# Kernel optimization log

Hardware: AMD Instinct MI355X
Metric: run time of the kernel (lower is better)

Reference implementation:

```python
import jax, jax.numpy as jnp
import numpy as np

L = 16384      # sequence length
D_IN = 512     # d_input
D_H = 1024     # d_hidden
D_OUT = 512    # d_output
R_MIN = 0.0
R_MAX = 0.99
MAX_PHASE = np.pi


def setup_inputs() -> dict:
    key = jax.random.key(0)
    k_nu, k_th, k_x, k_bre, k_bim, k_cre, k_cim, k_d = jax.random.split(key, 8)
    # nu_init with parametrization='exp'
    u_nu = jax.random.uniform(k_nu, (D_H,), dtype=jnp.float32)
    nu = jnp.sqrt(u_nu * (R_MAX ** 2 - R_MIN ** 2) + R_MIN ** 2)
    u_theta = jax.random.uniform(k_th, (D_H,), dtype=jnp.float32, minval=-MAX_PHASE, maxval=MAX_PHASE)
    theta = jnp.mod(u_theta, 2 * jnp.pi)
    lamb = jnp.stack([jnp.log(-jnp.log(nu)), jnp.log(theta)], axis=0)  # [2, D_H]
    # gamma_init with parametrization='exp': nu = exp(-exp(lamb[0]))
    nu_eff = jnp.exp(-jnp.exp(lamb[0]))
    gamma = jnp.log(jnp.sqrt(1.0 - jnp.abs(nu_eff) ** 2))  # [D_H]
    # matrix_init: normal / sqrt(shape[0])
    B_re = jax.random.normal(k_bre, (D_H, D_IN), dtype=jnp.float32) / jnp.sqrt(D_H)
    B_im = jax.random.normal(k_bim, (D_H, D_IN), dtype=jnp.float32) / jnp.sqrt(D_H)
    C_re = jax.random.normal(k_cre, (D_OUT, D_H), dtype=jnp.float32) / jnp.sqrt(D_OUT)
    C_im = jax.random.normal(k_cim, (D_OUT, D_H), dtype=jnp.float32) / jnp.sqrt(D_OUT)
    D = jax.random.normal(k_d, (D_OUT, D_IN), dtype=jnp.float32) / jnp.sqrt(D_OUT)
    inputs = jax.random.normal(k_x, (L, D_IN), dtype=jnp.float32)
    return {"inputs": inputs, "lamb": lamb, "gamma": gamma,
            "B_re": B_re, "B_im": B_im, "C_re": C_re, "C_im": C_im, "D": D}


def _binary_operator_diag(q_i, q_j):
    A_i, b_i = q_i
    A_j, b_j = q_j
    return (A_j * A_i, A_j * b_i + b_j)


def reference(inputs, lamb, gamma, B_re, B_im, C_re, C_im, D):
    # parametrization='exp': lambda = exp(-exp(nu_log) + i*exp(theta_log))
    diag_lambda = jnp.exp(-jnp.exp(lamb[0]) + 1j * jnp.exp(lamb[1]))  # [D_H] complex64
    # which_gamma='learned', exp param: scale rows of B by exp(gamma)
    B_norm = jnp.exp(gamma)[:, None] * (B_re + 1j * B_im)             # [D_H, D_IN]
    # Bu_t = B_norm @ x_t for all t, as one GEMM: [L, D_H] complex
    Bu = inputs.astype(B_norm.dtype) @ B_norm.T
    Lambda_elements = jnp.broadcast_to(diag_lambda[None, :], Bu.shape)
    # diagonal linear recurrence h_t = lambda*h_{t-1} + Bu_t via parallel scan
    _, h = jax.lax.associative_scan(_binary_operator_diag, (Lambda_elements, Bu))
    C = C_re + 1j * C_im
    # y_t = Re[C h_t] + D x_t
    outputs = jnp.real(h @ C.T) + inputs @ D.T  # [L, D_OUT]
    return outputs
```

## Files before the change

### kernel.cpp

```cpp
#include <hip/hip_runtime.h>

__device__ __forceinline__ unsigned short f2b(float f) {
    unsigned int u = __builtin_bit_cast(unsigned int, f);
    unsigned int r = (u + 0x7FFFu + ((u >> 16) & 1u)) >> 16;
    return (unsigned short)r;
}
__device__ __forceinline__ float b2f(unsigned short s) {
    unsigned int u = ((unsigned int)s) << 16;
    return __builtin_bit_cast(float, u);
}

typedef __attribute__((ext_vector_type(8))) short short8;
typedef __attribute__((ext_vector_type(4))) float float4v;

#define GLD16(g, l) __builtin_amdgcn_global_load_lds(                          \
    (const __attribute__((address_space(1))) unsigned int*)(g),                \
    (__attribute__((address_space(3))) unsigned int*)(l), 16, 0, 0)

#define WAIT_VMN(n)  __builtin_amdgcn_s_waitcnt(0x0F70 | (n))
#define SB()         __builtin_amdgcn_sched_barrier(0)
#define BAR()        __builtin_amdgcn_s_barrier()

#define SEQLEN 16384
#define NCHUNK 512
#define TCHUNK 32
#define LDH 2560

__global__ void prep_all(const float* __restrict__ x,
                         const float* __restrict__ B_re, const float* __restrict__ B_im,
                         const float* __restrict__ gamma,
                         const float* __restrict__ C_re, const float* __restrict__ C_im,
                         const float* __restrict__ Dm,
                         unsigned short* __restrict__ Hcat,
                         unsigned short* __restrict__ Bcat,
                         unsigned short* __restrict__ CW) {
    int b = blockIdx.x;
    if (b < 8192) {
        int id = b * 256 + threadIdx.x;
        int t = id >> 7;
        int k4 = (id & 127) << 2;
        float4 v = *(const float4*)(x + (long)t * 512 + k4);
        ushort4 o;
        o.x = f2b(v.x); o.y = f2b(v.y); o.z = f2b(v.z); o.w = f2b(v.w);
        *(ushort4*)(Hcat + (long)t * LDH + 2048 + k4) = o;
    } else if (b < 9216) {
        int id = (b - 8192) * 256 + threadIdx.x;
        int n = id >> 7;
        int k4 = (id & 127) << 2;
        const float* src = (n < 1024) ? (B_re + (long)n * 512) : (B_im + (long)(n - 1024) * 512);
        float g = expf(gamma[n & 1023]);
        float4 v = *(const float4*)(src + k4);
        ushort4 o;
        o.x = f2b(v.x * g); o.y = f2b(v.y * g); o.z = f2b(v.z * g); o.w = f2b(v.w * g);
        *(ushort4*)(Bcat + (long)n * 512 + k4) = o;
    } else {
        int id = (b - 9216) * 256 + threadIdx.x;
        int o = id / 640;
        int j4 = (id - o * 640) << 2;
        float4 v; float sgn = 1.0f;
        if (j4 < 1024) {
            v = *(const float4*)(C_re + (long)o * 1024 + j4);
        } else if (j4 < 2048) {
            v = *(const float4*)(C_im + (long)o * 1024 + (j4 - 1024));
            sgn = -1.0f;
        } else {
            v = *(const float4*)(Dm + (long)o * 512 + (j4 - 2048));
        }
        ushort4 w;
        w.x = f2b(v.x * sgn); w.y = f2b(v.y * sgn); w.z = f2b(v.z * sgn); w.w = f2b(v.w * sgn);
        *(ushort4*)(CW + (long)o * 2560 + j4) = w;
    }
}

__global__ __launch_bounds__(512, 1)
void gemm_bu(const unsigned short* __restrict__ A, int lda,
             const unsigned short* __restrict__ B, int ldb,
             unsigned short* __restrict__ Cout, int ldc) {
    constexpr int ASH = 16384;
    __shared__ unsigned short sm[2][32768] __attribute__((aligned(16)));

    const int tid  = threadIdx.x;
    const int lane = tid & 63;
    const int wid  = tid >> 6;
    const int wr   = wid >> 2;
    const int wc   = wid & 3;

    const int bid = blockIdx.x;
    const int l = (bid & 7) * 64 + (bid >> 3);
    const long m0 = (long)(l >> 3) * 256;
    const long n0 = (long)(l & 7) * 256;

    const int sr = lane >> 3;
    const int sc = ((lane & 7) ^ sr) << 3;
    const unsigned short* Agl = A + (m0 + sr) * (long)lda + sc;
    const unsigned short* Bgl = B + (n0 + sr) * (long)ldb + sc;

    const int fr = lane & 15;
    const int x7 = fr & 7;
    const int k0off = (((lane >> 4)    ) ^ x7) << 3;
    const int k1off = (((lane >> 4) + 4) ^ x7) << 3;

    float4v acc[8][4] = {};
    short8 fa[4][2];
    short8 fb[4][2];

    auto stageB = [&](unsigned short* buf, long kt) {
        unsigned short* ldsB = buf + ASH + wid * 512;
        const unsigned short* gB = Bgl + kt;
#pragma unroll
        for (int i = 0; i < 4; i++)
            GLD16(gB + (long)(8 * (wid + 8 * i)) * ldb, ldsB + i * 4096);
    };
    auto stageA = [&](unsigned short* buf, long kt) {
        unsigned short* ldsA = buf + wid * 512;
        const unsigned short* gA = Agl + kt;
#pragma unroll
        for (int i = 0; i < 4; i++)
            GLD16(gA + (long)(8 * (wid + 8 * i)) * lda, ldsA + i * 4096);
    };
    auto ldA = [&](const unsigned short* buf, int mbase) {
#pragma unroll
        for (int i = 0; i < 4; i++) {
            const unsigned short* p = buf + (wr * 128 + (mbase + i) * 16 + fr) * 64;
            fa[i][0] = *(const short8*)(p + k0off);
            fa[i][1] = *(const short8*)(p + k1off);
        }
    };
    auto ldB = [&](const unsigned short* buf, int nbase) {
#pragma unroll
        for (int j = 0; j < 2; j++) {
            const unsigned short* p = buf + ASH + (wc * 64 + (nbase + j) * 16 + fr) * 64;
            fb[nbase + j][0] = *(const short8*)(p + k0off);
            fb[nbase + j][1] = *(const short8*)(p + k1off);
        }
    };
    auto mfmaQ = [&](int mbase, int nbase) {
        __builtin_amdgcn_s_setprio(1);
#pragma unroll
        for (int i = 0; i < 4; i++)
#pragma unroll
            for (int j = 0; j < 2; j++) {
                acc[mbase + i][nbase + j] = __builtin_amdgcn_mfma_f32_16x16x32_bf16(
                    fa[i][0], fb[nbase + j][0], acc[mbase + i][nbase + j], 0, 0, 0);
                acc[mbase + i][nbase + j] = __builtin_amdgcn_mfma_f32_16x16x32_bf16(
                    fa[i][1], fb[nbase + j][1], acc[mbase + i][nbase + j], 0, 0, 0);
            }
        __builtin_amdgcn_s_setprio(0);
    };

    const int nk = 8;
    stageB(sm[0], 0);  stageA(sm[0], 0);
    stageB(sm[1], 64); stageA(sm[1], 64);
    WAIT_VMN(8);
    SB(); BAR(); SB();

    for (int t = 0; t < nk; ++t) {
        unsigned short* cur = sm[t & 1];
        const bool st = (t + 2 < nk);
        const long kt2 = (long)(t + 2) * 64;
        ldA(cur, 0); ldB(cur, 0);
        SB(); BAR(); SB();
        mfmaQ(0, 0);
        SB(); BAR(); SB();
        ldB(cur, 2);
        SB(); BAR(); SB();
        mfmaQ(0, 2);
        SB(); BAR(); SB();
        if (st) stageB(cur, kt2);
        ldA(cur, 4);
        SB(); BAR(); SB();
        mfmaQ(4, 0);
        SB(); BAR(); SB();
        if (st) stageA(cur, kt2);
        SB();
        mfmaQ(4, 2);
        if (st)              WAIT_VMN(8);
        else if (t + 1 < nk) WAIT_VMN(0);
        SB(); BAR(); SB();
    }

    const int er = (lane >> 4) * 4;
    const int ec = lane & 15;
#pragma unroll
    for (int mi = 0; mi < 8; mi++) {
#pragma unroll
        for (int r = 0; r < 4; r++) {
            long grow = m0 + wr * 128 + mi * 16 + er + r;
#pragma unroll
            for (int nj = 0; nj < 4; nj++) {
                long gcol = n0 + wc * 64 + nj * 16 + ec;
                Cout[grow * ldc + gcol] = f2b(acc[mi][nj][r]);
            }
        }
    }
}

__global__ __launch_bounds__(512, 1)
void gemm_y(const unsigned short* __restrict__ A, int lda,
            const unsigned short* __restrict__ B, int ldb,
            float* __restrict__ Cout, int ldc) {
    constexpr int ASH = 8192;
    __shared__ unsigned short sm[2][ASH + 16384] __attribute__((aligned(16)));

    const int tid  = threadIdx.x;
    const int lane = tid & 63;
    const int wid  = tid >> 6;
    const int wr   = wid >> 2;
    const int wc   = wid & 3;

    const int bid = blockIdx.x;
    const int xcd = bid & 7;
    const int g   = bid >> 3;
    const int bx  = g & 1;
    const int by  = xcd * 16 + (g >> 1);
    const long m0 = (long)by * 128;
    const long n0 = (long)bx * 256;

    const int sr = lane >> 3;
    const int sc = ((lane & 7) ^ sr) << 3;
    const unsigned short* Agl = A + (m0 + sr) * (long)lda + sc;
    const unsigned short* Bgl = B + (n0 + sr) * (long)ldb + sc;

    const int fr = lane & 15;
    const int x7 = fr & 7;
    const int k0off = (((lane >> 4)    ) ^ x7) << 3;
    const int k1off = (((lane >> 4) + 4) ^ x7) << 3;

    float4v acc[4][4] = {};
    short8 fa[2][2];
    short8 fb[4][2];

    auto stageB = [&](unsigned short* buf, long kt) {
        unsigned short* ldsB = buf + ASH + wid * 512;
        const unsigned short* gB = Bgl + kt;
#pragma unroll
        for (int i = 0; i < 4; i++)
            GLD16(gB + (long)(8 * (wid + 8 * i)) * ldb, ldsB + i * 4096);
    };
    auto stageA = [&](unsigned short* buf, long kt) {
        unsigned short* ldsA = buf + wid * 512;
        const unsigned short* gA = Agl + kt;
#pragma unroll
        for (int i = 0; i < 2; i++)
            GLD16(gA + (long)(8 * (wid + 8 * i)) * lda, ldsA + i * 4096);
    };
    auto ldA = [&](const unsigned short* buf, int mbase) {
#pragma unroll
        for (int i = 0; i < 2; i++) {
            const unsigned short* p = buf + (wr * 64 + (mbase + i) * 16 + fr) * 64;
            fa[i][0] = *(const short8*)(p + k0off);
            fa[i][1] = *(const short8*)(p + k1off);
        }
    };
    auto ldB = [&](const unsigned short* buf, int nbase) {
#pragma unroll
        for (int j = 0; j < 2; j++) {
            const unsigned short* p = buf + ASH + (wc * 64 + (nbase + j) * 16 + fr) * 64;
            fb[nbase + j][0] = *(const short8*)(p + k0off);
            fb[nbase + j][1] = *(const short8*)(p + k1off);
        }
    };
    auto mfmaQ = [&](int mbase, int nbase) {
        __builtin_amdgcn_s_setprio(1);
#pragma unroll
        for (int i = 0; i < 2; i++)
#pragma unroll
            for (int j = 0; j < 2; j++) {
                acc[mbase + i][nbase + j] = __builtin_amdgcn_mfma_f32_16x16x32_bf16(
                    fa[i][0], fb[nbase + j][0], acc[mbase + i][nbase + j], 0, 0, 0);
                acc[mbase + i][nbase + j] = __builtin_amdgcn_mfma_f32_16x16x32_bf16(
                    fa[i][1], fb[nbase + j][1], acc[mbase + i][nbase + j], 0, 0, 0);
            }
        __builtin_amdgcn_s_setprio(0);
    };

    const int nk = 40;
    stageB(sm[0], 0);  stageA(sm[0], 0);
    stageB(sm[1], 64); stageA(sm[1], 64);
    WAIT_VMN(6);
    SB(); BAR(); SB();

    for (int t = 0; t < nk; ++t) {
        unsigned short* cur = sm[t & 1];
        const bool st = (t + 2 < nk);
        const long kt2 = (long)(t + 2) * 64;
        ldA(cur, 0); ldB(cur, 0);
        SB(); BAR(); SB();
        mfmaQ(0, 0);
        SB(); BAR(); SB();
        ldB(cur, 2);
        SB(); BAR(); SB();
        mfmaQ(0, 2);
        SB(); BAR(); SB();
        if (st) stageB(cur, kt2);
        ldA(cur, 2);
        SB(); BAR(); SB();
        mfmaQ(2, 0);
        SB(); BAR(); SB();
        if (st) stageA(cur, kt2);
        SB();
        mfmaQ(2, 2);
        if (st)              WAIT_VMN(6);
        else if (t + 1 < nk) WAIT_VMN(0);
        SB(); BAR(); SB();
    }

    const int er = (lane >> 4) * 4;
    const int ec = lane & 15;
#pragma unroll
    for (int mi = 0; mi < 4; mi++) {
#pragma unroll
        for (int r = 0; r < 4; r++) {
            long grow = m0 + wr * 64 + mi * 16 + er + r;
#pragma unroll
            for (int nj = 0; nj < 4; nj++) {
                long gcol = n0 + wc * 64 + nj * 16 + ec;
                Cout[grow * ldc + gcol] = acc[mi][nj][r];
            }
        }
    }
}

__global__ void scan_ends(const unsigned short* __restrict__ Hcat,
                          const float* __restrict__ lamb,
                          float* __restrict__ E) {
    const int chunk = blockIdx.x;
    const int ch = threadIdx.x << 2;
    float lre[4], lim[4];
#pragma unroll
    for (int i = 0; i < 4; i++) {
        float nu = expf(-expf(lamb[ch + i]));
        float th = expf(lamb[1024 + ch + i]);
        lre[i] = nu * cosf(th);
        lim[i] = nu * sinf(th);
    }
    float hr[4] = {0, 0, 0, 0}, hi[4] = {0, 0, 0, 0};
    const unsigned short* base = Hcat + (long)chunk * TCHUNK * LDH + ch;
#pragma unroll 4
    for (int t = 0; t < TCHUNK; t++) {
        ushort4 br = *(const ushort4*)(base + (long)t * LDH);
        ushort4 bi = *(const ushort4*)(base + (long)t * LDH + 1024);
        float brf[4] = {b2f(br.x), b2f(br.y), b2f(br.z), b2f(br.w)};
        float bif[4] = {b2f(bi.x), b2f(bi.y), b2f(bi.z), b2f(bi.w)};
#pragma unroll
        for (int i = 0; i < 4; i++) {
            float nr = fmaf(lre[i], hr[i], fmaf(-lim[i], hi[i], brf[i]));
            float ni = fmaf(lre[i], hi[i], fmaf(lim[i], hr[i], bif[i]));
            hr[i] = nr; hi[i] = ni;
        }
    }
    float* Ec = E + (long)chunk * 2048 + ch;
#pragma unroll
    for (int i = 0; i < 4; i++) {
        Ec[i] = hr[i];
        Ec[1024 + i] = hi[i];
    }
}

__global__ void carry(const float* __restrict__ lamb, const float* __restrict__ E,
                      float* __restrict__ Kc) {
    const int lane = threadIdx.x & 63;
    const int ch = blockIdx.x * 4 + (threadIdx.x >> 6);
    double nu = exp(-exp((double)lamb[ch]));
    double th = exp((double)lamb[1024 + ch]);
    double lr = nu * cos(th), li = nu * sin(th);
#pragma unroll
    for (int i = 0; i < 5; i++) {
        double rr = lr * lr - li * li;
        double ii = 2.0 * lr * li;
        lr = rr; li = ii;
    }
    const float tre = (float)lr, tim = (float)li;
    double ar = lr, ai = li;
#pragma unroll
    for (int i = 0; i < 3; i++) {
        double rr = ar * ar - ai * ai;
        double ii = 2.0 * ar * ai;
        ar = rr; ai = ii;
    }
    float Ar = (float)ar, Ai = (float)ai;

    const int c0 = lane * 8;
    float er[8], ei[8];
#pragma unroll
    for (int j = 0; j < 8; j++) {
        er[j] = E[(long)(c0 + j) * 2048 + ch];
        ei[j] = E[(long)(c0 + j) * 2048 + 1024 + ch];
    }
    float hr = 0.0f, hi = 0.0f;
#pragma unroll
    for (int j = 0; j < 8; j++) {
        float nr = fmaf(tre, hr, fmaf(-tim, hi, er[j]));
        float ni = fmaf(tre, hi, fmaf(tim, hr, ei[j]));
        hr = nr; hi = ni;
    }
#pragma unroll
    for (int o = 1; o < 64; o <<= 1) {
        float pr = __shfl_up(hr, o);
        float pi = __shfl_up(hi, o);
        float qr = __shfl_up(Ar, o);
        float qi = __shfl_up(Ai, o);
        if (lane >= o) {
            float nr = fmaf(Ar, pr, fmaf(-Ai, pi, hr));
            float ni = fmaf(Ar, pi, fmaf(Ai, pr, hi));
            hr = nr; hi = ni;
            float nar = Ar * qr - Ai * qi;
            float nai = Ar * qi + Ai * qr;
            Ar = nar; Ai = nai;
        }
    }
    float sr = __shfl_up(hr, 1);
    float si = __shfl_up(hi, 1);
    if (lane == 0) { sr = 0.0f; si = 0.0f; }
#pragma unroll
    for (int j = 0; j < 8; j++) {
        Kc[(long)(c0 + j) * 2048 + ch] = sr;
        Kc[(long)(c0 + j) * 2048 + 1024 + ch] = si;
        float nr = fmaf(tre, sr, fmaf(-tim, si, er[j]));
        float ni = fmaf(tre, si, fmaf(tim, sr, ei[j]));
        sr = nr; si = ni;
    }
}

__global__ void scan_apply(unsigned short* __restrict__ Hcat,
                           const float* __restrict__ lamb,
                           const float* __restrict__ Kc) {
    const int chunk = blockIdx.x;
    const int ch = threadIdx.x << 2;
    float lre[4], lim[4];
#pragma unroll
    for (int i = 0; i < 4; i++) {
        float nu = expf(-expf(lamb[ch + i]));
        float th = expf(lamb[1024 + ch + i]);
        lre[i] = nu * cosf(th);
        lim[i] = nu * sinf(th);
    }
    float hr[4], hi[4];
#pragma unroll
    for (int i = 0; i < 4; i++) {
        hr[i] = Kc[(long)chunk * 2048 + ch + i];
        hi[i] = Kc[(long)chunk * 2048 + 1024 + ch + i];
    }
    unsigned short* base = Hcat + (long)chunk * TCHUNK * LDH + ch;
#pragma unroll 4
    for (int t = 0; t < TCHUNK; t++) {
        ushort4 br = *(const ushort4*)(base + (long)t * LDH);
        ushort4 bi = *(const ushort4*)(base + (long)t * LDH + 1024);
        float brf[4] = {b2f(br.x), b2f(br.y), b2f(br.z), b2f(br.w)};
        float bif[4] = {b2f(bi.x), b2f(bi.y), b2f(bi.z), b2f(bi.w)};
#pragma unroll
        for (int i = 0; i < 4; i++) {
            float nr = fmaf(lre[i], hr[i], fmaf(-lim[i], hi[i], brf[i]));
            float ni = fmaf(lre[i], hi[i], fmaf(lim[i], hr[i], bif[i]));
            hr[i] = nr; hi[i] = ni;
        }
        ushort4 orv, oiv;
        orv.x = f2b(hr[0]); orv.y = f2b(hr[1]); orv.z = f2b(hr[2]); orv.w = f2b(hr[3]);
        oiv.x = f2b(hi[0]); oiv.y = f2b(hi[1]); oiv.z = f2b(hi[2]); oiv.w = f2b(hi[3]);
        *(ushort4*)(base + (long)t * LDH) = orv;
        *(ushort4*)(base + (long)t * LDH + 1024) = oiv;
    }
}

extern "C" void kernel_launch(void* const* d_in, const int* in_sizes, int n_in,
                              void* d_out, int out_size, void* d_ws, size_t ws_size,
                              hipStream_t stream) {
    const float* x     = (const float*)d_in[0];
    const float* lamb  = (const float*)d_in[1];
    const float* gamma = (const float*)d_in[2];
    const float* B_re  = (const float*)d_in[3];
    const float* B_im  = (const float*)d_in[4];
    const float* C_re  = (const float*)d_in[5];
    const float* C_im  = (const float*)d_in[6];
    const float* Dm    = (const float*)d_in[7];

    char* ws = (char*)d_ws;
    unsigned short* Hcat = (unsigned short*)ws;
    float* E  = (float*)(ws + 83886080);
    float* Kc = E + (long)NCHUNK * 2048;
    unsigned short* Bcat = (unsigned short*)((char*)Kc + 4194304);
    unsigned short* CW   = Bcat + (long)2048 * 512;

    prep_all<<<10496, 256, 0, stream>>>(x, B_re, B_im, gamma, C_re, C_im, Dm,
                                        Hcat, Bcat, CW);
    gemm_bu<<<512, 512, 0, stream>>>(Hcat + 2048, LDH, Bcat, 512, Hcat, LDH);
    scan_ends<<<NCHUNK, 256, 0, stream>>>(Hcat, lamb, E);
    carry<<<256, 256, 0, stream>>>(lamb, E, Kc);
    scan_apply<<<NCHUNK, 256, 0, stream>>>(Hcat, lamb, Kc);
    gemm_y<<<256, 512, 0, stream>>>(Hcat, LDH, CW, 2560, (float*)d_out, 512);
}
```

Measured before the change: 234.2 us.

## Fuse chunk-end scan reduction into Bu GEMM epilogue via weighted sums

Removes the separate scan_ends kernel. The Bu GEMM tile is remapped so that each block holds matching real and imaginary channel columns. The block then computes each 32-step chunk's end state directly from its fp32 accumulators as a sum weighted by powers of lambda, combining the real and imaginary parts through LDS. This avoids re-reading the bf16 Hcat buffer and running a sequential loop per chunk. In exchange, the GEMM epilogue gains transcendental calls and extra barriers, and it uses unrounded fp32 values where the old path used bf16-rounded ones.

New measurement: 559.5 us. 2.39x slower.

```diff
diff --git a/kernel.cpp b/kernel.cpp
--- a/kernel.cpp
+++ b/kernel.cpp
@@ -75,7 +75,8 @@
 __global__ __launch_bounds__(512, 1)
 void gemm_bu(const unsigned short* __restrict__ A, int lda,
              const unsigned short* __restrict__ B, int ldb,
-             unsigned short* __restrict__ Cout, int ldc) {
+             unsigned short* __restrict__ Cout, int ldc,
+             float* __restrict__ Eout, const float* __restrict__ lamb) {
     constexpr int ASH = 16384;
     __shared__ unsigned short sm[2][32768] __attribute__((aligned(16)));
 
@@ -88,12 +89,11 @@
     const int bid = blockIdx.x;
     const int l = (bid & 7) * 64 + (bid >> 3);
     const long m0 = (long)(l >> 3) * 256;
-    const long n0 = (long)(l & 7) * 256;
+    const int  c0 = (l & 7) * 128;
 
     const int sr = lane >> 3;
     const int sc = ((lane & 7) ^ sr) << 3;
     const unsigned short* Agl = A + (m0 + sr) * (long)lda + sc;
-    const unsigned short* Bgl = B + (n0 + sr) * (long)ldb + sc;
 
     const int fr = lane & 15;
     const int x7 = fr & 7;
@@ -106,10 +106,13 @@
 
     auto stageB = [&](unsigned short* buf, long kt) {
         unsigned short* ldsB = buf + ASH + wid * 512;
-        const unsigned short* gB = Bgl + kt;
-#pragma unroll
-        for (int i = 0; i < 4; i++)
-            GLD16(gB + (long)(8 * (wid + 8 * i)) * ldb, ldsB + i * 4096);
+#pragma unroll
+        for (int i = 0; i < 4; i++) {
+            int q = wid + 8 * i;
+            long row8 = (q < 16) ? (long)(c0 + 8 * q)
+                                 : (long)(1024 + c0 + 8 * (q - 16));
+            GLD16(B + (row8 + sr) * (long)ldb + sc + kt, ldsB + i * 4096);
+        }
     };
     auto stageA = [&](unsigned short* buf, long kt) {
         unsigned short* ldsA = buf + wid * 512;
@@ -188,10 +191,73 @@
             long grow = m0 + wr * 128 + mi * 16 + er + r;
 #pragma unroll
             for (int nj = 0; nj < 4; nj++) {
-                long gcol = n0 + wc * 64 + nj * 16 + ec;
+                int col_local = wc * 64 + nj * 16 + ec;
+                long gcol = (col_local < 128) ? (long)(c0 + col_local)
+                                              : (long)(1024 + c0 + col_local - 128);
                 Cout[grow * ldc + gcol] = f2b(acc[mi][nj][r]);
             }
         }
+    }
+
+    float* Ls = (float*)(&sm[0][0]);
+    const int pairIdx = wr * 2 + (wc & 1);
+    const bool isIm = (wc >= 2);
+    const int by8 = (int)(l >> 3) * 8;
+#pragma unroll
+    for (int j = 0; j < 4; ++j) {
+        const int chj = c0 + (wc & 1) * 64 + j * 16 + ec;
+        const float e0 = expf(lamb[chj]);
+        const float th = expf(lamb[1024 + chj]);
+        float wRe[8], wIm[8];
+#pragma unroll
+        for (int sub = 0; sub < 2; ++sub)
+#pragma unroll
+            for (int r = 0; r < 4; ++r) {
+                float p = (float)(31 - sub * 16 - er - r);
+                float mag = expf(-p * e0);
+                float ang = p * th;
+                wRe[sub * 4 + r] = mag * cosf(ang);
+                wIm[sub * 4 + r] = mag * sinf(ang);
+            }
+        float S1[4], S2[4];
+#pragma unroll
+        for (int cc = 0; cc < 4; ++cc) {
+            S1[cc] = 0.0f; S2[cc] = 0.0f;
+#pragma unroll
+            for (int sub = 0; sub < 2; ++sub)
+#pragma unroll
+                for (int r = 0; r < 4; ++r) {
+                    float v = acc[cc * 2 + sub][j][r];
+                    S1[cc] = fmaf(wRe[sub * 4 + r], v, S1[cc]);
+                    S2[cc] = fmaf(wIm[sub * 4 + r], v, S2[cc]);
+                }
+        }
+#pragma unroll
+        for (int cc = 0; cc < 4; ++cc) {
+            S1[cc] += __shfl_xor(S1[cc], 16); S1[cc] += __shfl_xor(S1[cc], 32);
+            S2[cc] += __shfl_xor(S2[cc], 16); S2[cc] += __shfl_xor(S2[cc], 32);
+        }
+        if (isIm && lane < 16) {
+#pragma unroll
+            for (int cc = 0; cc < 4; ++cc) {
+                int slot = ((pairIdx * 4 + cc) * 16 + ec) * 2;
+                Ls[slot]     = S1[cc];
+                Ls[slot + 1] = S2[cc];
+            }
+        }
+        BAR();
+        if (!isIm && lane < 16) {
+#pragma unroll
+            for (int cc = 0; cc < 4; ++cc) {
+                int slot = ((pairIdx * 4 + cc) * 16 + ec) * 2;
+                float S3 = Ls[slot];
+                float S4 = Ls[slot + 1];
+                long g = by8 + wr * 4 + cc;
+                Eout[g * 2048 + chj]        = S1[cc] - S4;
+                Eout[g * 2048 + 1024 + chj] = S2[cc] + S3;
+            }
+        }
+        BAR();
     }
 }
 
@@ -318,42 +384,6 @@
                 Cout[grow * ldc + gcol] = acc[mi][nj][r];
             }
         }
-    }
-}
-
-__global__ void scan_ends(const unsigned short* __restrict__ Hcat,
-                          const float* __restrict__ lamb,
-                          float* __restrict__ E) {
-    const int chunk = blockIdx.x;
-    const int ch = threadIdx.x << 2;
-    float lre[4], lim[4];
-#pragma unroll
-    for (int i = 0; i < 4; i++) {
-        float nu = expf(-expf(lamb[ch + i]));
-        float th = expf(lamb[1024 + ch + i]);
-        lre[i] = nu * cosf(th);
-        lim[i] = nu * sinf(th);
-    }
-    float hr[4] = {0, 0, 0, 0}, hi[4] = {0, 0, 0, 0};
-    const unsigned short* base = Hcat + (long)chunk * TCHUNK * LDH + ch;
-#pragma unroll 4
-    for (int t = 0; t < TCHUNK; t++) {
-        ushort4 br = *(const ushort4*)(base + (long)t * LDH);
-        ushort4 bi = *(const ushort4*)(base + (long)t * LDH + 1024);
-        float brf[4] = {b2f(br.x), b2f(br.y), b2f(br.z), b2f(br.w)};
-        float bif[4] = {b2f(bi.x), b2f(bi.y), b2f(bi.z), b2f(bi.w)};
-#pragma unroll
-        for (int i = 0; i < 4; i++) {
-            float nr = fmaf(lre[i], hr[i], fmaf(-lim[i], hi[i], brf[i]));
-            float ni = fmaf(lre[i], hi[i], fmaf(lim[i], hr[i], bif[i]));
-            hr[i] = nr; hi[i] = ni;
-        }
-    }
-    float* Ec = E + (long)chunk * 2048 + ch;
-#pragma unroll
-    for (int i = 0; i < 4; i++) {
-        Ec[i] = hr[i];
-        Ec[1024 + i] = hi[i];
     }
 }
 
@@ -483,8 +513,7 @@
 
     prep_all<<<10496, 256, 0, stream>>>(x, B_re, B_im, gamma, C_re, C_im, Dm,
                                         Hcat, Bcat, CW);
-    gemm_bu<<<512, 512, 0, stream>>>(Hcat + 2048, LDH, Bcat, 512, Hcat, LDH);
-    scan_ends<<<NCHUNK, 256, 0, stream>>>(Hcat, lamb, E);
+    gemm_bu<<<512, 512, 0, stream>>>(Hcat + 2048, LDH, Bcat, 512, Hcat, LDH, E, lamb);
     carry<<<256, 256, 0, stream>>>(lamb, E, Kc);
     scan_apply<<<NCHUNK, 256, 0, stream>>>(Hcat, lamb, Kc);
     gemm_y<<<256, 512, 0, stream>>>(Hcat, LDH, CW, 2560, (float*)d_out, 512);
```

## Fuse chunk-end scan reduction into Bu GEMM epilogue via lambda-power weights

Applied to the files above, without the earlier changes.

Removes the scan_ends kernel. prep_all now builds a table of lambda^(31-t) weights, and the Bu GEMM epilogue uses it to compute each 32-step chunk's end state directly from fp32 accumulators, reducing across lanes with shuffles. Real and imaginary partial sums go to a 4096-wide per-chunk buffer that carry combines. This avoids re-reading the bf16 Hcat output for the chunk-end pass, at the cost of extra epilogue work and register pressure in the GEMM. It also changes numerics, since the end states now come from fp32 accumulators rather than bf16-rounded values.

Measured after the change: 237.3 us. Within noise of the previous version (+1.3%).

```diff
diff --git a/kernel.cpp b/kernel.cpp
--- a/kernel.cpp
+++ b/kernel.cpp
@@ -33,7 +33,9 @@
                          const float* __restrict__ Dm,
                          unsigned short* __restrict__ Hcat,
                          unsigned short* __restrict__ Bcat,
-                         unsigned short* __restrict__ CW) {
+                         unsigned short* __restrict__ CW,
+                         const float* __restrict__ lamb,
+                         float* __restrict__ Wtab) {
     int b = blockIdx.x;
     if (b < 8192) {
         int id = b * 256 + threadIdx.x;
@@ -53,7 +55,7 @@
         ushort4 o;
         o.x = f2b(v.x * g); o.y = f2b(v.y * g); o.z = f2b(v.z * g); o.w = f2b(v.w * g);
         *(ushort4*)(Bcat + (long)n * 512 + k4) = o;
-    } else {
+    } else if (b < 10496) {
         int id = (b - 9216) * 256 + threadIdx.x;
         int o = id / 640;
         int j4 = (id - o * 640) << 2;
@@ -69,13 +71,25 @@
         ushort4 w;
         w.x = f2b(v.x * sgn); w.y = f2b(v.y * sgn); w.z = f2b(v.z * sgn); w.w = f2b(v.w * sgn);
         *(ushort4*)(CW + (long)o * 2560 + j4) = w;
+    } else {
+        int id = (b - 10496) * 256 + threadIdx.x;
+        int t  = id >> 10;
+        int ch = id & 1023;
+        float p   = (float)(31 - t);
+        float e0  = expf(lamb[ch]);
+        float th  = expf(lamb[1024 + ch]);
+        float mag = expf(-p * e0);
+        float ang = p * th;
+        float2 w; w.x = mag * cosf(ang); w.y = mag * sinf(ang);
+        ((float2*)Wtab)[id] = w;
     }
 }
 
 __global__ __launch_bounds__(512, 1)
 void gemm_bu(const unsigned short* __restrict__ A, int lda,
              const unsigned short* __restrict__ B, int ldb,
-             unsigned short* __restrict__ Cout, int ldc) {
+             unsigned short* __restrict__ Cout, int ldc,
+             float* __restrict__ Epart, const float* __restrict__ Wtab) {
     constexpr int ASH = 16384;
     __shared__ unsigned short sm[2][32768] __attribute__((aligned(16)));
 
@@ -193,6 +207,40 @@
             }
         }
     }
+
+    const bool isIm = (n0 >= 1024);
+    const int pbase = isIm ? 2048 : 0;
+    const int by8 = (int)(m0 >> 5);
+    const float2* Wt = (const float2*)Wtab;
+#pragma unroll
+    for (int nj = 0; nj < 4; ++nj) {
+        const int ch = ((int)n0 + wc * 64 + nj * 16 + ec) & 1023;
+        float2 w[8];
+#pragma unroll
+        for (int sub = 0; sub < 2; ++sub)
+#pragma unroll
+            for (int r = 0; r < 4; ++r)
+                w[sub * 4 + r] = Wt[(sub * 16 + er + r) * 1024 + ch];
+#pragma unroll
+        for (int cc = 0; cc < 4; ++cc) {
+            float s1 = 0.0f, s2 = 0.0f;
+#pragma unroll
+            for (int sub = 0; sub < 2; ++sub)
+#pragma unroll
+                for (int r = 0; r < 4; ++r) {
+                    float v = acc[cc * 2 + sub][nj][r];
+                    s1 = fmaf(w[sub * 4 + r].x, v, s1);
+                    s2 = fmaf(w[sub * 4 + r].y, v, s2);
+                }
+            s1 += __shfl_xor(s1, 16); s1 += __shfl_xor(s1, 32);
+            s2 += __shfl_xor(s2, 16); s2 += __shfl_xor(s2, 32);
+            if (lane < 16) {
+                long g = by8 + wr * 4 + cc;
+                Epart[g * 4096 + pbase + ch]        = s1;
+                Epart[g * 4096 + pbase + 1024 + ch] = s2;
+            }
+        }
+    }
 }
 
 __global__ __launch_bounds__(512, 1)
@@ -321,43 +369,7 @@
     }
 }
 
-__global__ void scan_ends(const unsigned short* __restrict__ Hcat,
-                          const float* __restrict__ lamb,
-                          float* __restrict__ E) {
-    const int chunk = blockIdx.x;
-    const int ch = threadIdx.x << 2;
-    float lre[4], lim[4];
-#pragma unroll
-    for (int i = 0; i < 4; i++) {
-        float nu = expf(-expf(lamb[ch + i]));
-        float th = expf(lamb[1024 + ch + i]);
-        lre[i] = nu * cosf(th);
-        lim[i] = nu * sinf(th);
-    }
-    float hr[4] = {0, 0, 0, 0}, hi[4] = {0, 0, 0, 0};
-    const unsigned short* base = Hcat + (long)chunk * TCHUNK * LDH + ch;
-#pragma unroll 4
-    for (int t = 0; t < TCHUNK; t++) {
-        ushort4 br = *(const ushort4*)(base + (long)t * LDH);
-        ushort4 bi = *(const ushort4*)(base + (long)t * LDH + 1024);
-        float brf[4] = {b2f(br.x), b2f(br.y), b2f(br.z), b2f(br.w)};
-        float bif[4] = {b2f(bi.x), b2f(bi.y), b2f(bi.z), b2f(bi.w)};
-#pragma unroll
-        for (int i = 0; i < 4; i++) {
-            float nr = fmaf(lre[i], hr[i], fmaf(-lim[i], hi[i], brf[i]));
-            float ni = fmaf(lre[i], hi[i], fmaf(lim[i], hr[i], bif[i]));
-            hr[i] = nr; hi[i] = ni;
-        }
-    }
-    float* Ec = E + (long)chunk * 2048 + ch;
-#pragma unroll
-    for (int i = 0; i < 4; i++) {
-        Ec[i] = hr[i];
-        Ec[1024 + i] = hi[i];
-    }
-}
-
-__global__ void carry(const float* __restrict__ lamb, const float* __restrict__ E,
+__global__ void carry(const float* __restrict__ lamb, const float* __restrict__ Ep,
                       float* __restrict__ Kc) {
     const int lane = threadIdx.x & 63;
     const int ch = blockIdx.x * 4 + (threadIdx.x >> 6);
@@ -384,8 +396,9 @@
     float er[8], ei[8];
 #pragma unroll
     for (int j = 0; j < 8; j++) {
-        er[j] = E[(long)(c0 + j) * 2048 + ch];
-        ei[j] = E[(long)(c0 + j) * 2048 + 1024 + ch];
+        const float* p = Ep + (long)(c0 + j) * 4096;
+        er[j] = p[ch] - p[3072 + ch];
+        ei[j] = p[1024 + ch] + p[2048 + ch];
     }
     float hr = 0.0f, hi = 0.0f;
 #pragma unroll
@@ -476,16 +489,16 @@
 
     char* ws = (char*)d_ws;
     unsigned short* Hcat = (unsigned short*)ws;
-    float* E  = (float*)(ws + 83886080);
-    float* Kc = E + (long)NCHUNK * 2048;
+    float* Epart = (float*)(ws + 83886080);
+    float* Kc    = Epart + (long)NCHUNK * 4096;
     unsigned short* Bcat = (unsigned short*)((char*)Kc + 4194304);
     unsigned short* CW   = Bcat + (long)2048 * 512;
-
-    prep_all<<<10496, 256, 0, stream>>>(x, B_re, B_im, gamma, C_re, C_im, Dm,
-                                        Hcat, Bcat, CW);
-    gemm_bu<<<512, 512, 0, stream>>>(Hcat + 2048, LDH, Bcat, 512, Hcat, LDH);
-    scan_ends<<<NCHUNK, 256, 0, stream>>>(Hcat, lamb, E);
-    carry<<<256, 256, 0, stream>>>(lamb, E, Kc);
+    float* Wtab = (float*)((char*)CW + 2621440);
+
+    prep_all<<<10624, 256, 0, stream>>>(x, B_re, B_im, gamma, C_re, C_im, Dm,
+                                        Hcat, Bcat, CW, lamb, Wtab);
+    gemm_bu<<<512, 512, 0, stream>>>(Hcat + 2048, LDH, Bcat, 512, Hcat, LDH, Epart, Wtab);
+    carry<<<256, 256, 0, stream>>>(lamb, Epart, Kc);
     scan_apply<<<NCHUNK, 256, 0, stream>>>(Hcat, lamb, Kc);
     gemm_y<<<256, 512, 0, stream>>>(Hcat, LDH, CW, 2560, (float*)d_out, 512);
 }
```
